# Kernel optimization log

Measured on AMD Instinct MI355X. Metric: run time of the kernel, lower is better.

## Reference

```python
import jax, jax.numpy as jnp
import numpy as np

B, J, HID, INTER, NL = 4096, 16, 128, 64, 4
NEG = -9.0e15
EDGES = [(0,1),(1,2),(2,3),(0,4),(4,5),(5,6),(0,7),(7,8),(8,9),(8,10),(10,11),(11,12),(8,13),(13,14),(14,15)]
GROUPED = [0,7,1,4,2,5,3,6,8,10,9,13,11,14,12,15]  # flattened nodes_group


def _adjacency_nonzeros():
    A = np.zeros((J, J), np.float32)
    for i, j in EDGES:
        A[i, j] = 1.0
        A[j, i] = 1.0
    A += np.eye(J, dtype=np.float32)
    rows, cols = np.nonzero(A)  # row-major, matches torch adj[mask] = e fill order
    return rows.astype(np.int32), cols.astype(np.int32)


def setup_inputs() -> dict:
    key = jax.random.key(0)
    ks = iter(jax.random.split(key, 64))
    rn = lambda shape, s: jax.random.normal(next(ks), shape, jnp.float32) * s
    rows, cols = _adjacency_nonzeros()
    nnz = rows.shape[0]  # 46
    inp = dict(
        x=jax.random.normal(next(ks), (B, J, 2), jnp.float32),
        # input SemGraphConv (2 -> HID) + its BatchNorm
        gc_in_W=rn((2, 2, HID), 0.7), gc_in_e=1.0 + rn((nnz,), 0.3), gc_in_b=rn((HID,), 0.05),
        bn_in_g=1.0 + rn((HID,), 0.05), bn_in_b=rn((HID,), 0.05),
        # 4 residual blocks x 2 graph convs (HID -> HID)
        W_res=rn((2 * NL, 2, HID, HID), 0.08), e_res=1.0 + rn((2 * NL, nnz), 0.3),
        b_res=rn((2 * NL, HID), 0.05),
        bng_res=1.0 + rn((2 * NL, HID), 0.05), bnb_res=rn((2 * NL, HID), 0.05),
        # 5 GraphNonLocal blocks (1 after input + 1 per residual block)
        nl_g_w=rn((NL + 1, INTER, HID), 0.08), nl_g_b=rn((NL + 1, INTER), 0.05),
        nl_t_w=rn((NL + 1, INTER, HID), 0.08), nl_t_b=rn((NL + 1, INTER), 0.05),
        nl_p_w=rn((NL + 1, INTER, HID), 0.08), nl_p_b=rn((NL + 1, INTER), 0.05),
        nl_cp_w=rn((NL + 1, 2 * INTER), 0.08),  # concat_project 1x1 conv, no bias
        nl_W_w=rn((NL + 1, HID, INTER), 0.08), nl_W_b=rn((NL + 1, HID), 0.05),
        nl_bn_g=1.0 + rn((NL + 1, HID), 0.05), nl_bn_b=rn((NL + 1, HID), 0.05),
        # output SemGraphConv (HID -> 3)
        gc_out_W=rn((2, HID, 3), 0.08), gc_out_e=1.0 + rn((nnz,), 0.3), gc_out_b=rn((3,), 0.05),
        # integer constants
        mask_rows=jnp.asarray(rows), mask_cols=jnp.asarray(cols),
        grouped_order=jnp.asarray(GROUPED, jnp.int32),
        restored_order=jnp.asarray(np.argsort(GROUPED), jnp.int32),
    )
    return inp


def reference(x, gc_in_W, gc_in_e, gc_in_b, bn_in_g, bn_in_b,
              W_res, e_res, b_res, bng_res, bnb_res,
              nl_g_w, nl_g_b, nl_t_w, nl_t_b, nl_p_w, nl_p_b,
              nl_cp_w, nl_W_w, nl_W_b, nl_bn_g, nl_bn_b,
              gc_out_W, gc_out_e, gc_out_b,
              mask_rows, mask_cols, grouped_order, restored_order):
    eye = jnp.eye(J, dtype=x.dtype)

    def gconv(h, W, e, b):
        # h: [B, J, F]
        h0 = jnp.einsum('bjf,fo->bjo', h, W[0])
        h1 = jnp.einsum('bjf,fo->bjo', h, W[1])
        logits = jnp.full((J, J), NEG, h.dtype).at[mask_rows, mask_cols].set(e)
        adj = jax.nn.softmax(logits, axis=1)
        diag = jnp.diagonal(adj)                     # adj*I picks diagonal scaling
        off = adj * (1.0 - eye)
        return diag[None, :, None] * h0 + jnp.einsum('ij,bjo->bio', off, h1) + b

    def bn(h, g, bta, axes):
        # training-mode BatchNorm (biased variance), per-channel
        m = h.mean(axes, keepdims=True)
        v = h.var(axes, keepdims=True)
        return (h - m) * jax.lax.rsqrt(v + 1e-5) * g + bta

    def graph_conv(h, W, e, b, gm, gb):
        h = gconv(h, W, e, b)
        h = bn(h, gm[None, None, :], gb[None, None, :], (0, 1))
        return jax.nn.relu(h)

    def nonlocal_block(h, i):
        xo = h[:, grouped_order]          # [B, J, C] regroup joints
        xc = xo.transpose(0, 2, 1)        # [B, C, J]
        conv = lambda w, bb: jnp.einsum('oc,bcj->boj', w, xc) + bb[None, :, None]
        pool = lambda t: t.reshape(B, INTER, J // 2, 2).max(-1)   # MaxPool1d(k=2)
        gx = pool(conv(nl_g_w[i], nl_g_b[i]))                     # [B, I, J/2]
        th = conv(nl_t_w[i], nl_t_b[i])                           # [B, I, J]
        ph = pool(conv(nl_p_w[i], nl_p_b[i]))                     # [B, I, J/2]
        wt, wp = nl_cp_w[i][:INTER], nl_cp_w[i][INTER:]
        # concat_project 1x1 conv over concat(theta,phi) decomposes into a sum
        f = jax.nn.relu(jnp.einsum('bch,c->bh', th, wt)[:, :, None]
                        + jnp.einsum('bcw,c->bw', ph, wp)[:, None, :])  # [B, J, J/2]
        f = f / (J // 2)
        y = jnp.einsum('bhw,bcw->bch', f, gx)                     # [B, I, J]
        Wy = jnp.einsum('oc,bch->boh', nl_W_w[i], y) + nl_W_b[i][None, :, None]
        Wy = bn(Wy, nl_bn_g[i][None, :, None], nl_bn_b[i][None, :, None], (0, 2))
        z = Wy + xc
        return z.transpose(0, 2, 1)[:, restored_order]

    out = graph_conv(x, gc_in_W, gc_in_e, gc_in_b, bn_in_g, bn_in_b)
    out = nonlocal_block(out, 0)
    for i in range(NL):
        res = out
        out = graph_conv(out, W_res[2 * i], e_res[2 * i], b_res[2 * i], bng_res[2 * i], bnb_res[2 * i])
        out = graph_conv(out, W_res[2 * i + 1], e_res[2 * i + 1], b_res[2 * i + 1], bng_res[2 * i + 1], bnb_res[2 * i + 1])
        out = res + out
        out = nonlocal_block(out, i + 1)
    return gconv(out, gc_out_W, gc_out_e, gc_out_b)  # [B, J, 3]
```

## Files before the change

kernel.cpp:

```cpp
#include <hip/hip_runtime.h>

#define B 4096
#define J 16
#define HID 128
#define INTER 64
#define NLAYERS 4
#define NEGV -9000000000000000.0f
#define ELEMS ((size_t)B*16*128)
#define NREP 16
#define SLOT 4096

typedef __attribute__((ext_vector_type(8))) short short8;
typedef __attribute__((ext_vector_type(4))) float f32x4;

static __device__ __forceinline__ unsigned short f2bf(float x) {
    unsigned u = __float_as_uint(x);
    unsigned r = u + 0x7fffu + ((u >> 16) & 1u);
    return (unsigned short)(r >> 16);
}
static __device__ __forceinline__ void splitbf(float x, unsigned short& h, unsigned short& l) {
    h = f2bf(x);
    float hf = __uint_as_float((unsigned)h << 16);
    l = f2bf(x - hf);
}
static __device__ __forceinline__ void splitbf4(float4 v, uint2& hh, uint2& ll) {
    unsigned short h0,l0,h1,l1,h2,l2,h3,l3;
    splitbf(v.x,h0,l0); splitbf(v.y,h1,l1); splitbf(v.z,h2,l2); splitbf(v.w,h3,l3);
    hh = make_uint2((unsigned)h0 | ((unsigned)h1<<16), (unsigned)h2 | ((unsigned)h3<<16));
    ll = make_uint2((unsigned)l0 | ((unsigned)l1<<16), (unsigned)l2 | ((unsigned)l3<<16));
}
static __device__ __forceinline__ f32x4 mfma16(short8 a, short8 b, f32x4 c) {
    return __builtin_amdgcn_mfma_f32_16x16x32_bf16(a, b, c, 0, 0, 0);
}
static __device__ __forceinline__ f32x4 mfma_split(short8 ah, short8 al,
                                                   short8 bh, short8 bl, f32x4 acc) {
    acc = mfma16(ah, bh, acc);
    acc = mfma16(ah, bl, acc);
    acc = mfma16(al, bh, acc);
    return acc;
}
static __device__ __forceinline__ float bfpair(unsigned short h, unsigned short l) {
    return __uint_as_float((unsigned)h << 16) + __uint_as_float((unsigned)l << 16);
}

__global__ void adj_kernel(const float* __restrict__ e_in,
                           const float* __restrict__ e_res,
                           const float* __restrict__ e_out,
                           const int* __restrict__ rows,
                           const int* __restrict__ cols, int nnz,
                           float* __restrict__ off_all,
                           float* __restrict__ diag_all) {
    int m = blockIdx.x;
    int i = threadIdx.x;
    const float* e = (m == 0) ? e_in : (m <= 8) ? e_res + (size_t)(m - 1) * nnz : e_out;
    float l[16];
    for (int j = 0; j < 16; j++) l[j] = NEGV;
    for (int k = 0; k < nnz; k++)
        if (rows[k] == i) l[cols[k]] = e[k];
    float mx = l[0];
    for (int j = 1; j < 16; j++) mx = fmaxf(mx, l[j]);
    float ex[16], s = 0.f;
    for (int j = 0; j < 16; j++) { ex[j] = expf(l[j] - mx); s += ex[j]; }
    float inv = 1.f / s;
    for (int j = 0; j < 16; j++) {
        float a = ex[j] * inv;
        if (j == i) { diag_all[m * 16 + i] = a; a = 0.f; }
        off_all[m * 256 + i * 16 + j] = a;
    }
}

#define WB_N   262144
#define NLW_N  122880
#define NLWW_N 40960
__global__ void prep_w_kernel(const float* __restrict__ W_res,
                              const float* __restrict__ g_w, const float* __restrict__ t_w,
                              const float* __restrict__ p_w, const float* __restrict__ W_w,
                              unsigned short* __restrict__ Wbh, unsigned short* __restrict__ Wbl,
                              unsigned short* __restrict__ nlwh, unsigned short* __restrict__ nlwl,
                              unsigned short* __restrict__ nlWh, unsigned short* __restrict__ nlWl) {
    int i = blockIdx.x * 256 + threadIdx.x;
    unsigned short h, l;
    if (i < WB_N) {
        int lay = i >> 15, rem = i & 32767, n = rem >> 8, k = rem & 255;
        int d = k >> 7, f = k & 127;
        splitbf(W_res[(((lay << 1) | d) * 128 + f) * 128 + n], h, l);
        Wbh[i] = h; Wbl[i] = l;
    } else if (i < WB_N + NLW_N) {
        int j = i - WB_N;
        int lay = j / 24576, r2 = j % 24576;
        int conv = r2 >> 13, oc = r2 & 8191;
        const float* src = conv == 0 ? g_w : conv == 1 ? t_w : p_w;
        splitbf(src[lay * 8192 + oc], h, l);
        nlwh[j] = h; nlwl[j] = l;
    } else if (i < WB_N + NLW_N + NLWW_N) {
        int j = i - WB_N - NLW_N;
        splitbf(W_w[j], h, l);
        nlWh[j] = h; nlWl[j] = l;
    }
}

__global__ void prep_vt_kernel(const float* __restrict__ t_w, const float* __restrict__ t_b,
                               const float* __restrict__ cp_w,
                               float* __restrict__ vt, float* __restrict__ ct) {
    int l = blockIdx.x, c = threadIdx.x;
    float s = 0.f;
    for (int c2 = 0; c2 < 64; c2++)
        s += cp_w[l * 128 + c2] * t_w[(l * 64 + c2) * 128 + c];
    vt[l * 128 + c] = s;
    if (c == 0) {
        float s2 = 0.f;
        for (int c2 = 0; c2 < 64; c2++) s2 += cp_w[l * 128 + c2] * t_b[l * 64 + c2];
        ct[l] = s2;
    }
}

__global__ void finalize_kernel(const float* __restrict__ slot, float* __restrict__ fin) {
    __shared__ float sh[256];
    int t = threadIdx.x;
    float s = 0.f;
    #pragma unroll
    for (int r = 0; r < NREP; r++) s += slot[r * 256 + t];
    sh[t] = s;
    __syncthreads();
    if (t < 128) {
        float m = sh[t] * (1.f / 65536.f);
        float v = sh[128 + t] * (1.f / 65536.f) - m * m;
        fin[t] = m;
        fin[128 + t] = rsqrtf(v + 1e-5f);
    }
}

__global__ __launch_bounds__(256) void gconv_in_kernel(
        const float* __restrict__ x, const float* __restrict__ W,
        const float* __restrict__ bias, const float* __restrict__ off,
        const float* __restrict__ diag, float* __restrict__ out,
        float* __restrict__ stats_out) {
    __shared__ float xs[16][2];
    __shared__ float gs[16][2];
    __shared__ float red[512];
    int b = blockIdx.x, t = threadIdx.x;
    if (t < 32) xs[t >> 1][t & 1] = x[b * 32 + t];
    __syncthreads();
    if (t < 32) {
        int i = t >> 1, f = t & 1;
        float g = 0.f;
        #pragma unroll
        for (int j = 0; j < 16; j++) g += off[i * 16 + j] * xs[j][f];
        gs[i][f] = g;
    }
    __syncthreads();
    int o = t & 127;
    float w00 = W[o], w01 = W[128 + o], w10 = W[256 + o], w11 = W[384 + o], bo = bias[o];
    float s = 0.f, q = 0.f;
    for (int idx = t; idx < 2048; idx += 256) {
        int i = idx >> 7;
        float v = diag[i] * (xs[i][0] * w00 + xs[i][1] * w01)
                + gs[i][0] * w10 + gs[i][1] * w11 + bo;
        out[(size_t)b * 2048 + idx] = v;
        s += v; q += v * v;
    }
    red[t] = s; red[256 + t] = q;
    __syncthreads();
    float* so = stats_out + (b & (NREP - 1)) * 256;
    if (t < 128) {
        atomicAdd(&so[t], red[t] + red[t + 128]);
        atomicAdd(&so[128 + t], red[256 + t] + red[256 + t + 128]);
    }
}

__global__ __launch_bounds__(256) void gconv_mfma_kernel(
        const float* src, const float* wy,
        const float* __restrict__ fin,
        const float* __restrict__ bn_g, const float* __restrict__ bn_b,
        const int* __restrict__ restored, float* zdst,
        const unsigned short* __restrict__ Wbh,
        const unsigned short* __restrict__ Wbl,
        const float* __restrict__ bias,
        const float* __restrict__ off, const float* __restrict__ diag,
        float* dst, float* __restrict__ stats_out) {
    __shared__ float hraw[16][132];
    __shared__ __align__(16) unsigned short ksh[16][264];
    __shared__ __align__(16) unsigned short ksl[16][264];
    __shared__ float offs[256];
    __shared__ float diags[16];
    int t = threadIdx.x;
    offs[t] = off[t];
    if (t < 16) diags[t] = diag[t];
    int c4 = (4 * t) & 127;
    int r0 = t >> 5;
    float4 m4 = make_float4(0,0,0,0), sc4 = make_float4(0,0,0,0), bb4 = make_float4(0,0,0,0);
    if (fin) {
        m4 = *(const float4*)&fin[c4];
        float4 iv = *(const float4*)&fin[128 + c4];
        float4 g4 = *(const float4*)&bn_g[c4];
        bb4 = *(const float4*)&bn_b[c4];
        sc4 = make_float4(iv.x * g4.x, iv.y * g4.y, iv.z * g4.z, iv.w * g4.w);
    }
    int ro0 = 0, ro1 = 0;
    if (wy) { ro0 = restored[r0]; ro1 = restored[r0 + 8]; }
    int b0 = blockIdx.x;
    const float4* src4 = (const float4*)src;
    const float4* wy4  = (const float4*)wy;
    float4 sv0 = src4[(size_t)b0 * 512 + t];
    float4 sv1 = src4[(size_t)b0 * 512 + 256 + t];
    float4 wv0 = make_float4(0,0,0,0), wv1 = make_float4(0,0,0,0);
    if (wy) {
        wv0 = wy4[(size_t)b0 * 512 + ro0 * 32 + (c4 >> 2)];
        wv1 = wy4[(size_t)b0 * 512 + ro1 * 32 + (c4 >> 2)];
    }
    int wv_ = t >> 6, lane = t & 63;
    int mn = lane & 15, kq = (lane >> 4) << 3, qr = (lane >> 4) << 2;

    for (int s = 0; s < 2; s++) {
        int bb_ = blockIdx.x + s * 2048;
        {
            float4 v = sv0;
            if (wy) {
                v.x += (wv0.x - m4.x) * sc4.x + bb4.x;
                v.y += (wv0.y - m4.y) * sc4.y + bb4.y;
                v.z += (wv0.z - m4.z) * sc4.z + bb4.z;
                v.w += (wv0.w - m4.w) * sc4.w + bb4.w;
                ((float4*)zdst)[(size_t)bb_ * 512 + t] = v;
            } else if (fin) {
                v.x = fmaxf((v.x - m4.x) * sc4.x + bb4.x, 0.f);
                v.y = fmaxf((v.y - m4.y) * sc4.y + bb4.y, 0.f);
                v.z = fmaxf((v.z - m4.z) * sc4.z + bb4.z, 0.f);
                v.w = fmaxf((v.w - m4.w) * sc4.w + bb4.w, 0.f);
            }
            *(float4*)&hraw[r0][c4] = v;
            v = sv1;
            if (wy) {
                v.x += (wv1.x - m4.x) * sc4.x + bb4.x;
                v.y += (wv1.y - m4.y) * sc4.y + bb4.y;
                v.z += (wv1.z - m4.z) * sc4.z + bb4.z;
                v.w += (wv1.w - m4.w) * sc4.w + bb4.w;
                ((float4*)zdst)[(size_t)bb_ * 512 + 256 + t] = v;
            } else if (fin) {
                v.x = fmaxf((v.x - m4.x) * sc4.x + bb4.x, 0.f);
                v.y = fmaxf((v.y - m4.y) * sc4.y + bb4.y, 0.f);
                v.z = fmaxf((v.z - m4.z) * sc4.z + bb4.z, 0.f);
                v.w = fmaxf((v.w - m4.w) * sc4.w + bb4.w, 0.f);
            }
            *(float4*)&hraw[r0 + 8][c4] = v;
        }
        if (s == 0) {
            int b1 = blockIdx.x + 2048;
            sv0 = src4[(size_t)b1 * 512 + t];
            sv1 = src4[(size_t)b1 * 512 + 256 + t];
            if (wy) {
                wv0 = wy4[(size_t)b1 * 512 + ro0 * 32 + (c4 >> 2)];
                wv1 = wy4[(size_t)b1 * 512 + ro1 * 32 + (c4 >> 2)];
            }
        }
        __syncthreads();
        for (int u = t; u < 512; u += 256) {
            int i = u >> 5, f4 = (u & 31) << 2;
            float4 hv = *(const float4*)&hraw[i][f4];
            float4 g = make_float4(0.f, 0.f, 0.f, 0.f);
            #pragma unroll
            for (int j = 0; j < 16; j++) {
                float w = offs[i * 16 + j];
                float4 hj = *(const float4*)&hraw[j][f4];
                g.x += w * hj.x; g.y += w * hj.y; g.z += w * hj.z; g.w += w * hj.w;
            }
            float d = diags[i];
            uint2 hh, ll;
            splitbf4(make_float4(d * hv.x, d * hv.y, d * hv.z, d * hv.w), hh, ll);
            *(uint2*)&ksh[i][f4] = hh;
            *(uint2*)&ksl[i][f4] = ll;
            splitbf4(g, hh, ll);
            *(uint2*)&ksh[i][128 + f4] = hh;
            *(uint2*)&ksl[i][128 + f4] = ll;
        }
        __syncthreads();
        int n0 = wv_ << 5;
        f32x4 acc0 = {0.f, 0.f, 0.f, 0.f}, acc1 = {0.f, 0.f, 0.f, 0.f};
        const unsigned short* wh0 = Wbh + (size_t)(n0 + mn) * 256 + kq;
        const unsigned short* wl0 = Wbl + (size_t)(n0 + mn) * 256 + kq;
        #pragma unroll
        for (int k = 0; k < 8; k++) {
            int k0 = k << 5;
            short8 ah = *(const short8*)&ksh[mn][k0 + kq];
            short8 al = *(const short8*)&ksl[mn][k0 + kq];
            acc0 = mfma_split(ah, al, *(const short8*)(wh0 + k0), *(const short8*)(wl0 + k0), acc0);
            acc1 = mfma_split(ah, al, *(const short8*)(wh0 + 4096 + k0), *(const short8*)(wl0 + 4096 + k0), acc1);
        }
        float bias0 = bias[n0 + mn], bias1 = bias[n0 + 16 + mn];
        float s0 = 0.f, q0 = 0.f, s1 = 0.f, q1 = 0.f;
        #pragma unroll
        for (int r = 0; r < 4; r++) {
            int row = qr + r;
            float v0 = acc0[r] + bias0;
            float v1 = acc1[r] + bias1;
            dst[(size_t)bb_ * 2048 + row * 128 + n0 + mn] = v0;
            dst[(size_t)bb_ * 2048 + row * 128 + n0 + 16 + mn] = v1;
            s0 += v0; q0 += v0 * v0; s1 += v1; q1 += v1 * v1;
        }
        s0 += __shfl_xor(s0, 16); s0 += __shfl_xor(s0, 32);
        q0 += __shfl_xor(q0, 16); q0 += __shfl_xor(q0, 32);
        s1 += __shfl_xor(s1, 16); s1 += __shfl_xor(s1, 32);
        q1 += __shfl_xor(q1, 16); q1 += __shfl_xor(q1, 32);
        float* so = stats_out + (bb_ & (NREP - 1)) * 256;
        if (lane < 16) {
            atomicAdd(&so[n0 + mn], s0);
            atomicAdd(&so[128 + n0 + mn], q0);
            atomicAdd(&so[n0 + 16 + mn], s1);
            atomicAdd(&so[128 + n0 + 16 + mn], q1);
        }
        if (s == 0) __syncthreads();
    }
}

#define CG(conv, o, j) cgbuf[((conv) * 64 + (o)) * 17 + (j)]
#define WYL(o, j)      cgbuf[(o) * 17 + (j)]
__global__ __launch_bounds__(512) void nl_a_kernel(
        const float* tsrc, const float* __restrict__ fin,
        const float* __restrict__ bn_g, const float* __restrict__ bn_b,
        const float* res,
        const unsigned short* __restrict__ nlwh,
        const unsigned short* __restrict__ nlwl,
        const float* __restrict__ g_b, const float* __restrict__ p_b,
        const float* __restrict__ cpw,
        const float* __restrict__ vt, const float* __restrict__ ctp,
        const unsigned short* __restrict__ nlWh,
        const unsigned short* __restrict__ nlWl,
        const float* __restrict__ W_b,
        const int* __restrict__ restored,
        float* hdst, float* wydst, float* __restrict__ wst) {
    __shared__ __align__(16) unsigned short xch[16][136];
    __shared__ __align__(16) unsigned short xcl[16][136];
    __shared__ float cgbuf[2176];
    __shared__ float gx[64][9];
    __shared__ float tvp[16][4], pvp[8][8];
    __shared__ float tv[16], pv[8];
    __shared__ float vtl[128];
    __shared__ __align__(16) unsigned short ybh[16][72];
    __shared__ __align__(16) unsigned short ybl[16][72];
    __shared__ float redS[512], redQ[512];
    int b = blockIdx.x, t = threadIdx.x;
    {
        if (t < 128) vtl[t] = vt[t];
        int c4 = (4 * t) & 127;
        int r = t >> 5;
        float4 m4 = *(const float4*)&fin[c4];
        float4 iv = *(const float4*)&fin[128 + c4];
        float4 g4 = *(const float4*)&bn_g[c4];
        float4 bb4 = *(const float4*)&bn_b[c4];
        float4 sc4 = make_float4(iv.x * g4.x, iv.y * g4.y, iv.z * g4.z, iv.w * g4.w);
        float4 v = ((const float4*)tsrc)[(size_t)b * 512 + t];
        v.x = fmaxf((v.x - m4.x) * sc4.x + bb4.x, 0.f);
        v.y = fmaxf((v.y - m4.y) * sc4.y + bb4.y, 0.f);
        v.z = fmaxf((v.z - m4.z) * sc4.z + bb4.z, 0.f);
        v.w = fmaxf((v.w - m4.w) * sc4.w + bb4.w, 0.f);
        if (res) {
            float4 rv = ((const float4*)res)[(size_t)b * 512 + t];
            v.x += rv.x; v.y += rv.y; v.z += rv.z; v.w += rv.w;
        }
        ((float4*)hdst)[(size_t)b * 512 + t] = v;
        int rg = restored[r];
        uint2 hh, ll;
        splitbf4(v, hh, ll);
        *(uint2*)&xch[rg][c4] = hh;
        *(uint2*)&xcl[rg][c4] = ll;
    }
    __syncthreads();
    int w = t >> 6, lane = t & 63;
    int mn = lane & 15, kq = (lane >> 4) << 3, qr = (lane >> 4) << 2;
    {
        int conv = w >> 2;
        int mt = w & 3;
        int wbase = (conv == 0) ? 0 : 128;
        const unsigned short* aph = nlwh + (size_t)(wbase + mt * 16 + mn) * 128 + kq;
        const unsigned short* apl = nlwl + (size_t)(wbase + mt * 16 + mn) * 128 + kq;
        f32x4 acc = {0.f, 0.f, 0.f, 0.f};
        #pragma unroll
        for (int k = 0; k < 4; k++) {
            short8 bh = *(const short8*)&xch[mn][k * 32 + kq];
            short8 bl = *(const short8*)&xcl[mn][k * 32 + kq];
            acc = mfma_split(*(const short8*)(aph + k * 32), *(const short8*)(apl + k * 32),
                             bh, bl, acc);
        }
        const float* bias = (conv == 0) ? g_b : p_b;
        #pragma unroll
        for (int r = 0; r < 4; r++) {
            int o = mt * 16 + qr + r;
            CG(conv, o, mn) = acc[r] + bias[o];
        }
    }
    __syncthreads();
    {
        int c = t >> 3, w2 = t & 7;
        gx[c][w2] = fmaxf(CG(0, c, 2 * w2), CG(0, c, 2 * w2 + 1));
        if (t < 64) {
            int w2b = t & 7, ch = t >> 3;
            float ss = 0.f;
            for (int cc = ch * 8; cc < ch * 8 + 8; cc++)
                ss += fmaxf(CG(1, cc, 2 * w2b), CG(1, cc, 2 * w2b + 1)) * cpw[64 + cc];
            pvp[w2b][ch] = ss;
        } else if (t < 128) {
            int u = t - 64, j = u & 15, ch = u >> 4;
            float ss = 0.f;
            int c0 = ch * 32;
            for (int cc = c0; cc < c0 + 32; cc += 2) {
                unsigned hh = *(const unsigned*)&xch[j][cc];
                unsigned ll = *(const unsigned*)&xcl[j][cc];
                float v0 = bfpair((unsigned short)hh, (unsigned short)ll);
                float v1 = bfpair((unsigned short)(hh >> 16), (unsigned short)(ll >> 16));
                ss += vtl[cc] * v0 + vtl[cc + 1] * v1;
            }
            tvp[j][ch] = ss;
        }
    }
    __syncthreads();
    if (t < 16) {
        tv[t] = tvp[t][0] + tvp[t][1] + tvp[t][2] + tvp[t][3] + ctp[0];
    } else if (t < 24) {
        int w2 = t - 16;
        float ss = 0.f;
        #pragma unroll
        for (int ch = 0; ch < 8; ch++) ss += pvp[w2][ch];
        pv[w2] = ss;
    }
    __syncthreads();
    #pragma unroll
    for (int u2 = 0; u2 < 2; u2++) {
        int u = t + u2 * 512;
        int j = u >> 6, c = u & 63;
        float ss = 0.f;
        #pragma unroll
        for (int w2 = 0; w2 < 8; w2++)
            ss += fmaxf(tv[j] + pv[w2], 0.f) * gx[c][w2];
        unsigned short h, l;
        splitbf(ss * 0.125f, h, l);
        ybh[j][c] = h; ybl[j][c] = l;
    }
    __syncthreads();
    {
        int mt = w;
        short8 byh0 = *(const short8*)&ybh[mn][kq];
        short8 byh1 = *(const short8*)&ybh[mn][32 + kq];
        short8 byl0 = *(const short8*)&ybl[mn][kq];
        short8 byl1 = *(const short8*)&ybl[mn][32 + kq];
        const unsigned short* aph = nlWh + (size_t)(mt * 16 + mn) * 64 + kq;
        const unsigned short* apl = nlWl + (size_t)(mt * 16 + mn) * 64 + kq;
        f32x4 acc = {0.f, 0.f, 0.f, 0.f};
        acc = mfma_split(*(const short8*)aph, *(const short8*)apl, byh0, byl0, acc);
        acc = mfma_split(*(const short8*)(aph + 32), *(const short8*)(apl + 32), byh1, byl1, acc);
        #pragma unroll
        for (int r = 0; r < 4; r++) {
            int o = mt * 16 + qr + r;
            WYL(o, mn) = acc[r] + W_b[o];
        }
    }
    __syncthreads();
    {
        int c = t & 127;
        float ss = 0.f, qq = 0.f;
        #pragma unroll
        for (int u2 = 0; u2 < 4; u2++) {
            int idx = t + u2 * 512;
            int j = idx >> 7;
            float v = WYL(c, j);
            wydst[(size_t)b * 2048 + idx] = v;
            ss += v; qq += v * v;
        }
        redS[t] = ss; redQ[t] = qq;
        __syncthreads();
        float* so = wst + (b & (NREP - 1)) * 256;
        if (t < 128) {
            float s4 = redS[t] + redS[t + 128] + redS[t + 256] + redS[t + 384];
            float q4 = redQ[t] + redQ[t + 128] + redQ[t + 256] + redQ[t + 384];
            atomicAdd(&so[t], s4);
            atomicAdd(&so[128 + t], q4);
        }
    }
}

__global__ __launch_bounds__(256) void gconv_out_kernel(
        const float* __restrict__ h, const float* __restrict__ wy,
        const float* __restrict__ fin,
        const float* __restrict__ nlg, const float* __restrict__ nlb,
        const int* __restrict__ restored,
        const float* __restrict__ W,
        const float* __restrict__ bias, const float* __restrict__ off,
        const float* __restrict__ diag, float* __restrict__ out) {
    __shared__ float hs[16][132];
    __shared__ float gsv[16][132];
    __shared__ float offs[256];
    __shared__ float p0[48][4], p1[48][4];
    int b = blockIdx.x, t = threadIdx.x;
    offs[t] = off[t];
    {
        int c = t & 127;
        float mean = fin[c];
        float inv = fin[128 + c] * nlg[c];
        float bb = nlb[c];
        for (int idx = t; idx < 2048; idx += 256) {
            int r = idx >> 7;
            float wval = wy[(size_t)b * 2048 + restored[r] * 128 + c];
            hs[r][c] = (wval - mean) * inv + bb + h[(size_t)b * 2048 + idx];
        }
    }
    __syncthreads();
    for (int idx = t; idx < 2048; idx += 256) {
        int i = idx >> 7, f = idx & 127;
        float g = 0.f;
        #pragma unroll
        for (int j = 0; j < 16; j++) g += offs[i * 16 + j] * hs[j][f];
        gsv[i][f] = g;
    }
    __syncthreads();
    if (t < 192) {
        int oid = t >> 2, chunk = t & 3;
        int i = oid / 3, o = oid % 3;
        float a0 = 0.f, a1 = 0.f;
        int f0 = chunk * 32;
        for (int f = f0; f < f0 + 32; f++) {
            a0 += hs[i][f] * W[f * 3 + o];
            a1 += gsv[i][f] * W[384 + f * 3 + o];
        }
        p0[oid][chunk] = a0; p1[oid][chunk] = a1;
    }
    __syncthreads();
    if (t < 48) {
        int i = t / 3, o = t % 3;
        float a0 = p0[t][0] + p0[t][1] + p0[t][2] + p0[t][3];
        float a1 = p1[t][0] + p1[t][1] + p1[t][2] + p1[t][3];
        out[(size_t)b * 48 + t] = diag[i] * a0 + a1 + bias[o];
    }
}

extern "C" void kernel_launch(void* const* d_in, const int* in_sizes, int n_in,
                              void* d_out, int out_size, void* d_ws, size_t ws_size,
                              hipStream_t stream) {
    (void)n_in; (void)out_size; (void)ws_size;
    const float* x        = (const float*)d_in[0];
    const float* gc_in_W  = (const float*)d_in[1];
    const float* gc_in_e  = (const float*)d_in[2];
    const float* gc_in_b  = (const float*)d_in[3];
    const float* bn_in_g  = (const float*)d_in[4];
    const float* bn_in_b  = (const float*)d_in[5];
    const float* W_res    = (const float*)d_in[6];
    const float* e_res    = (const float*)d_in[7];
    const float* b_res    = (const float*)d_in[8];
    const float* bng_res  = (const float*)d_in[9];
    const float* bnb_res  = (const float*)d_in[10];
    const float* nl_g_w   = (const float*)d_in[11];
    const float* nl_g_b   = (const float*)d_in[12];
    const float* nl_t_w   = (const float*)d_in[13];
    const float* nl_t_b   = (const float*)d_in[14];
    const float* nl_p_w   = (const float*)d_in[15];
    const float* nl_p_b   = (const float*)d_in[16];
    const float* nl_cp_w  = (const float*)d_in[17];
    const float* nl_W_w   = (const float*)d_in[18];
    const float* nl_W_b   = (const float*)d_in[19];
    const float* nl_bn_g  = (const float*)d_in[20];
    const float* nl_bn_b  = (const float*)d_in[21];
    const float* gc_out_W = (const float*)d_in[22];
    const float* gc_out_e = (const float*)d_in[23];
    const float* gc_out_b = (const float*)d_in[24];
    const int*   mask_rows = (const int*)d_in[25];
    const int*   mask_cols = (const int*)d_in[26];
    const int*   restored  = (const int*)d_in[28];
    int nnz = in_sizes[2];

    float* ws       = (float*)d_ws;
    float* off_all  = ws;
    float* diag_all = ws + 2560;
    float* stats    = ws + 2720;
    float* fin      = ws + 60064;
    float* vt       = ws + 63664;
    float* ct       = ws + 64304;
    unsigned short* Wbh  = (unsigned short*)(ws + 65536);
    unsigned short* Wbl  = Wbh + WB_N;
    unsigned short* nlwh = Wbl + WB_N;
    unsigned short* nlwl = nlwh + NLW_N;
    unsigned short* nlWh = nlwl + NLW_N;
    unsigned short* nlWl = nlWh + NLWW_N;
    float* Z = ws + 491520;
    float* T = Z + ELEMS;

    hipMemsetAsync(stats, 0, 14 * SLOT * sizeof(float), stream);
    adj_kernel<<<10, 16, 0, stream>>>(gc_in_e, e_res, gc_out_e, mask_rows, mask_cols,
                                      nnz, off_all, diag_all);
    prep_w_kernel<<<(WB_N + NLW_N + NLWW_N + 255) / 256, 256, 0, stream>>>(
        W_res, nl_g_w, nl_t_w, nl_p_w, nl_W_w, Wbh, Wbl, nlwh, nlwl, nlWh, nlWl);
    prep_vt_kernel<<<5, 128, 0, stream>>>(nl_t_w, nl_t_b, nl_cp_w, vt, ct);

    gconv_in_kernel<<<B, 256, 0, stream>>>(x, gc_in_W, gc_in_b, off_all, diag_all,
                                           T, stats);
    finalize_kernel<<<1, 256, 0, stream>>>(stats, fin);
    nl_a_kernel<<<B, 512, 0, stream>>>(T, fin, bn_in_g, bn_in_b, nullptr,
                                       nlwh, nlwl, nl_g_b, nl_p_b, nl_cp_w,
                                       vt, ct, nlWh, nlWl, nl_W_b, restored,
                                       Z, T, stats + SLOT);
    finalize_kernel<<<1, 256, 0, stream>>>(stats + SLOT, fin + 256);

    int sl = 1;
    for (int i = 0; i < NLAYERS; i++) {
        int l0 = 2 * i, l1 = 2 * i + 1, li = i + 1;
        gconv_mfma_kernel<<<2048, 256, 0, stream>>>(
            Z, T, fin + (size_t)sl * 256,
            nl_bn_g + i * 128, nl_bn_b + i * 128, restored, Z,
            Wbh + (size_t)l0 * 32768, Wbl + (size_t)l0 * 32768, b_res + l0 * 128,
            off_all + (1 + l0) * 256, diag_all + (1 + l0) * 16, T,
            stats + (size_t)(sl + 1) * SLOT);
        finalize_kernel<<<1, 256, 0, stream>>>(stats + (size_t)(sl + 1) * SLOT,
                                               fin + (size_t)(sl + 1) * 256);
        gconv_mfma_kernel<<<2048, 256, 0, stream>>>(
            T, nullptr, fin + (size_t)(sl + 1) * 256,
            bng_res + l0 * 128, bnb_res + l0 * 128, nullptr, nullptr,
            Wbh + (size_t)l1 * 32768, Wbl + (size_t)l1 * 32768, b_res + l1 * 128,
            off_all + (1 + l1) * 256, diag_all + (1 + l1) * 16, T,
            stats + (size_t)(sl + 2) * SLOT);
        finalize_kernel<<<1, 256, 0, stream>>>(stats + (size_t)(sl + 2) * SLOT,
                                               fin + (size_t)(sl + 2) * 256);
        nl_a_kernel<<<B, 512, 0, stream>>>(
            T, fin + (size_t)(sl + 2) * 256,
            bng_res + l1 * 128, bnb_res + l1 * 128, Z,
            nlwh + li * 24576, nlwl + li * 24576,
            nl_g_b + li * 64, nl_p_b + li * 64, nl_cp_w + li * 128,
            vt + li * 128, ct + li, nlWh + li * 8192, nlWl + li * 8192,
            nl_W_b + li * 128, restored, Z, T,
            stats + (size_t)(sl + 3) * SLOT);
        finalize_kernel<<<1, 256, 0, stream>>>(stats + (size_t)(sl + 3) * SLOT,
                                               fin + (size_t)(sl + 3) * 256);
        sl += 3;
    }
    gconv_out_kernel<<<B, 256, 0, stream>>>(Z, T, fin + (size_t)sl * 256,
                                            nl_bn_g + NLAYERS * 128, nl_bn_b + NLAYERS * 128,
                                            restored, gc_out_W, gc_out_b,
                                            off_all + 9 * 256, diag_all + 9 * 16,
                                            (float*)d_out);
}
```

Before: 901.7 us.

## Process one batch sample per 512-thread block in graph conv kernel

```diff
diff --git a/kernel.cpp b/kernel.cpp
--- a/kernel.cpp
+++ b/kernel.cpp
@@ -168,7 +168,7 @@
     }
 }
 
-__global__ __launch_bounds__(256) void gconv_mfma_kernel(
+__global__ __launch_bounds__(512) void gconv_mfma_kernel(
         const float* src, const float* wy,
         const float* __restrict__ fin,
         const float* __restrict__ bn_g, const float* __restrict__ bn_b,
@@ -183,131 +183,86 @@
     __shared__ __align__(16) unsigned short ksl[16][264];
     __shared__ float offs[256];
     __shared__ float diags[16];
-    int t = threadIdx.x;
-    offs[t] = off[t];
-    if (t < 16) diags[t] = diag[t];
+    int b = blockIdx.x, t = threadIdx.x;
+    if (t < 256) offs[t] = off[t];
+    if (t >= 256 && t < 272) diags[t - 256] = diag[t - 256];
     int c4 = (4 * t) & 127;
     int r0 = t >> 5;
-    float4 m4 = make_float4(0,0,0,0), sc4 = make_float4(0,0,0,0), bb4 = make_float4(0,0,0,0);
-    if (fin) {
-        m4 = *(const float4*)&fin[c4];
-        float4 iv = *(const float4*)&fin[128 + c4];
-        float4 g4 = *(const float4*)&bn_g[c4];
-        bb4 = *(const float4*)&bn_b[c4];
-        sc4 = make_float4(iv.x * g4.x, iv.y * g4.y, iv.z * g4.z, iv.w * g4.w);
-    }
-    int ro0 = 0, ro1 = 0;
-    if (wy) { ro0 = restored[r0]; ro1 = restored[r0 + 8]; }
-    int b0 = blockIdx.x;
-    const float4* src4 = (const float4*)src;
-    const float4* wy4  = (const float4*)wy;
-    float4 sv0 = src4[(size_t)b0 * 512 + t];
-    float4 sv1 = src4[(size_t)b0 * 512 + 256 + t];
-    float4 wv0 = make_float4(0,0,0,0), wv1 = make_float4(0,0,0,0);
-    if (wy) {
-        wv0 = wy4[(size_t)b0 * 512 + ro0 * 32 + (c4 >> 2)];
-        wv1 = wy4[(size_t)b0 * 512 + ro1 * 32 + (c4 >> 2)];
-    }
-    int wv_ = t >> 6, lane = t & 63;
+    {
+        float4 m4 = make_float4(0,0,0,0), sc4 = make_float4(0,0,0,0), bb4 = make_float4(0,0,0,0);
+        if (fin) {
+            m4 = *(const float4*)&fin[c4];
+            float4 iv = *(const float4*)&fin[128 + c4];
+            float4 g4 = *(const float4*)&bn_g[c4];
+            bb4 = *(const float4*)&bn_b[c4];
+            sc4 = make_float4(iv.x * g4.x, iv.y * g4.y, iv.z * g4.z, iv.w * g4.w);
+        }
+        float4 v = ((const float4*)src)[(size_t)b * 512 + t];
+        if (wy) {
+            int ro = restored[r0];
+            float4 wv = ((const float4*)wy)[(size_t)b * 512 + ro * 32 + (c4 >> 2)];
+            v.x += (wv.x - m4.x) * sc4.x + bb4.x;
+            v.y += (wv.y - m4.y) * sc4.y + bb4.y;
+            v.z += (wv.z - m4.z) * sc4.z + bb4.z;
+            v.w += (wv.w - m4.w) * sc4.w + bb4.w;
+            ((float4*)zdst)[(size_t)b * 512 + t] = v;
+        } else if (fin) {
+            v.x = fmaxf((v.x - m4.x) * sc4.x + bb4.x, 0.f);
+            v.y = fmaxf((v.y - m4.y) * sc4.y + bb4.y, 0.f);
+            v.z = fmaxf((v.z - m4.z) * sc4.z + bb4.z, 0.f);
+            v.w = fmaxf((v.w - m4.w) * sc4.w + bb4.w, 0.f);
+        }
+        *(float4*)&hraw[r0][c4] = v;
+    }
+    __syncthreads();
+    {
+        int i = t >> 5, f4 = (t & 31) << 2;
+        float4 hv = *(const float4*)&hraw[i][f4];
+        float4 g = make_float4(0.f, 0.f, 0.f, 0.f);
+        #pragma unroll
+        for (int j = 0; j < 16; j++) {
+            float w = offs[i * 16 + j];
+            float4 hj = *(const float4*)&hraw[j][f4];
+            g.x += w * hj.x; g.y += w * hj.y; g.z += w * hj.z; g.w += w * hj.w;
+        }
+        float d = diags[i];
+        uint2 hh, ll;
+        splitbf4(make_float4(d * hv.x, d * hv.y, d * hv.z, d * hv.w), hh, ll);
+        *(uint2*)&ksh[i][f4] = hh;
+        *(uint2*)&ksl[i][f4] = ll;
+        splitbf4(g, hh, ll);
+        *(uint2*)&ksh[i][128 + f4] = hh;
+        *(uint2*)&ksl[i][128 + f4] = ll;
+    }
+    __syncthreads();
+    int w = t >> 6, lane = t & 63;
     int mn = lane & 15, kq = (lane >> 4) << 3, qr = (lane >> 4) << 2;
-
-    for (int s = 0; s < 2; s++) {
-        int bb_ = blockIdx.x + s * 2048;
-        {
-            float4 v = sv0;
-            if (wy) {
-                v.x += (wv0.x - m4.x) * sc4.x + bb4.x;
-                v.y += (wv0.y - m4.y) * sc4.y + bb4.y;
-                v.z += (wv0.z - m4.z) * sc4.z + bb4.z;
-                v.w += (wv0.w - m4.w) * sc4.w + bb4.w;
-                ((float4*)zdst)[(size_t)bb_ * 512 + t] = v;
-            } else if (fin) {
-                v.x = fmaxf((v.x - m4.x) * sc4.x + bb4.x, 0.f);
-                v.y = fmaxf((v.y - m4.y) * sc4.y + bb4.y, 0.f);
-                v.z = fmaxf((v.z - m4.z) * sc4.z + bb4.z, 0.f);
-                v.w = fmaxf((v.w - m4.w) * sc4.w + bb4.w, 0.f);
-            }
-            *(float4*)&hraw[r0][c4] = v;
-            v = sv1;
-            if (wy) {
-                v.x += (wv1.x - m4.x) * sc4.x + bb4.x;
-                v.y += (wv1.y - m4.y) * sc4.y + bb4.y;
-                v.z += (wv1.z - m4.z) * sc4.z + bb4.z;
-                v.w += (wv1.w - m4.w) * sc4.w + bb4.w;
-                ((float4*)zdst)[(size_t)bb_ * 512 + 256 + t] = v;
-            } else if (fin) {
-                v.x = fmaxf((v.x - m4.x) * sc4.x + bb4.x, 0.f);
-                v.y = fmaxf((v.y - m4.y) * sc4.y + bb4.y, 0.f);
-                v.z = fmaxf((v.z - m4.z) * sc4.z + bb4.z, 0.f);
-                v.w = fmaxf((v.w - m4.w) * sc4.w + bb4.w, 0.f);
-            }
-            *(float4*)&hraw[r0 + 8][c4] = v;
-        }
-        if (s == 0) {
-            int b1 = blockIdx.x + 2048;
-            sv0 = src4[(size_t)b1 * 512 + t];
-            sv1 = src4[(size_t)b1 * 512 + 256 + t];
-            if (wy) {
-                wv0 = wy4[(size_t)b1 * 512 + ro0 * 32 + (c4 >> 2)];
-                wv1 = wy4[(size_t)b1 * 512 + ro1 * 32 + (c4 >> 2)];
-            }
-        }
-        __syncthreads();
-        for (int u = t; u < 512; u += 256) {
-            int i = u >> 5, f4 = (u & 31) << 2;
-            float4 hv = *(const float4*)&hraw[i][f4];
-            float4 g = make_float4(0.f, 0.f, 0.f, 0.f);
-            #pragma unroll
-            for (int j = 0; j < 16; j++) {
-                float w = offs[i * 16 + j];
-                float4 hj = *(const float4*)&hraw[j][f4];
-                g.x += w * hj.x; g.y += w * hj.y; g.z += w * hj.z; g.w += w * hj.w;
-            }
-            float d = diags[i];
-            uint2 hh, ll;
-            splitbf4(make_float4(d * hv.x, d * hv.y, d * hv.z, d * hv.w), hh, ll);
-            *(uint2*)&ksh[i][f4] = hh;
-            *(uint2*)&ksl[i][f4] = ll;
-            splitbf4(g, hh, ll);
-            *(uint2*)&ksh[i][128 + f4] = hh;
-            *(uint2*)&ksl[i][128 + f4] = ll;
-        }
-        __syncthreads();
-        int n0 = wv_ << 5;
-        f32x4 acc0 = {0.f, 0.f, 0.f, 0.f}, acc1 = {0.f, 0.f, 0.f, 0.f};
-        const unsigned short* wh0 = Wbh + (size_t)(n0 + mn) * 256 + kq;
-        const unsigned short* wl0 = Wbl + (size_t)(n0 + mn) * 256 + kq;
-        #pragma unroll
-        for (int k = 0; k < 8; k++) {
-            int k0 = k << 5;
-            short8 ah = *(const short8*)&ksh[mn][k0 + kq];
-            short8 al = *(const short8*)&ksl[mn][k0 + kq];
-            acc0 = mfma_split(ah, al, *(const short8*)(wh0 + k0), *(const short8*)(wl0 + k0), acc0);
-            acc1 = mfma_split(ah, al, *(const short8*)(wh0 + 4096 + k0), *(const short8*)(wl0 + 4096 + k0), acc1);
-        }
-        float bias0 = bias[n0 + mn], bias1 = bias[n0 + 16 + mn];
-        float s0 = 0.f, q0 = 0.f, s1 = 0.f, q1 = 0.f;
-        #pragma unroll
-        for (int r = 0; r < 4; r++) {
-            int row = qr + r;
-            float v0 = acc0[r] + bias0;
-            float v1 = acc1[r] + bias1;
-            dst[(size_t)bb_ * 2048 + row * 128 + n0 + mn] = v0;
-            dst[(size_t)bb_ * 2048 + row * 128 + n0 + 16 + mn] = v1;
-            s0 += v0; q0 += v0 * v0; s1 += v1; q1 += v1 * v1;
-        }
-        s0 += __shfl_xor(s0, 16); s0 += __shfl_xor(s0, 32);
-        q0 += __shfl_xor(q0, 16); q0 += __shfl_xor(q0, 32);
-        s1 += __shfl_xor(s1, 16); s1 += __shfl_xor(s1, 32);
-        q1 += __shfl_xor(q1, 16); q1 += __shfl_xor(q1, 32);
-        float* so = stats_out + (bb_ & (NREP - 1)) * 256;
-        if (lane < 16) {
-            atomicAdd(&so[n0 + mn], s0);
-            atomicAdd(&so[128 + n0 + mn], q0);
-            atomicAdd(&so[n0 + 16 + mn], s1);
-            atomicAdd(&so[128 + n0 + 16 + mn], q1);
-        }
-        if (s == 0) __syncthreads();
+    int n0 = w << 4;
+    f32x4 acc = {0.f, 0.f, 0.f, 0.f};
+    const unsigned short* wh0 = Wbh + (size_t)(n0 + mn) * 256 + kq;
+    const unsigned short* wl0 = Wbl + (size_t)(n0 + mn) * 256 + kq;
+    #pragma unroll
+    for (int k = 0; k < 8; k++) {
+        int k0 = k << 5;
+        short8 ah = *(const short8*)&ksh[mn][k0 + kq];
+        short8 al = *(const short8*)&ksl[mn][k0 + kq];
+        acc = mfma_split(ah, al, *(const short8*)(wh0 + k0), *(const short8*)(wl0 + k0), acc);
+    }
+    float bo = bias[n0 + mn];
+    float s0 = 0.f, q0 = 0.f;
+    #pragma unroll
+    for (int r = 0; r < 4; r++) {
+        int row = qr + r;
+        float v0 = acc[r] + bo;
+        dst[(size_t)b * 2048 + row * 128 + n0 + mn] = v0;
+        s0 += v0; q0 += v0 * v0;
+    }
+    s0 += __shfl_xor(s0, 16); s0 += __shfl_xor(s0, 32);
+    q0 += __shfl_xor(q0, 16); q0 += __shfl_xor(q0, 32);
+    float* so = stats_out + (b & (NREP - 1)) * 256;
+    if (lane < 16) {
+        atomicAdd(&so[n0 + mn], s0);
+        atomicAdd(&so[128 + n0 + mn], q0);
     }
 }
 
@@ -599,7 +554,7 @@
     int sl = 1;
     for (int i = 0; i < NLAYERS; i++) {
         int l0 = 2 * i, l1 = 2 * i + 1, li = i + 1;
-        gconv_mfma_kernel<<<2048, 256, 0, stream>>>(
+        gconv_mfma_kernel<<<B, 512, 0, stream>>>(
             Z, T, fin + (size_t)sl * 256,
             nl_bn_g + i * 128, nl_bn_b + i * 128, restored, Z,
             Wbh + (size_t)l0 * 32768, Wbl + (size_t)l0 * 32768, b_res + l0 * 128,
@@ -607,7 +562,7 @@
             stats + (size_t)(sl + 1) * SLOT);
         finalize_kernel<<<1, 256, 0, stream>>>(stats + (size_t)(sl + 1) * SLOT,
                                                fin + (size_t)(sl + 1) * 256);
-        gconv_mfma_kernel<<<2048, 256, 0, stream>>>(
+        gconv_mfma_kernel<<<B, 512, 0, stream>>>(
             T, nullptr, fin + (size_t)(sl + 1) * 256,
             bng_res + l0 * 128, bnb_res + l0 * 128, nullptr, nullptr,
             Wbh + (size_t)l1 * 32768, Wbl + (size_t)l1 * 32768, b_res + l1 * 128,
```

New measurement: 1.093 ms. +21.3%, slower.

## Process two batch samples per nl_a block with prefetch of the next input

Applied to the files above, without the earlier changes.

```diff
diff --git a/kernel.cpp b/kernel.cpp
--- a/kernel.cpp
+++ b/kernel.cpp
@@ -337,141 +337,152 @@
     __shared__ __align__(16) unsigned short ybh[16][72];
     __shared__ __align__(16) unsigned short ybl[16][72];
     __shared__ float redS[512], redQ[512];
-    int b = blockIdx.x, t = threadIdx.x;
-    {
-        if (t < 128) vtl[t] = vt[t];
-        int c4 = (4 * t) & 127;
-        int r = t >> 5;
-        float4 m4 = *(const float4*)&fin[c4];
-        float4 iv = *(const float4*)&fin[128 + c4];
-        float4 g4 = *(const float4*)&bn_g[c4];
-        float4 bb4 = *(const float4*)&bn_b[c4];
-        float4 sc4 = make_float4(iv.x * g4.x, iv.y * g4.y, iv.z * g4.z, iv.w * g4.w);
-        float4 v = ((const float4*)tsrc)[(size_t)b * 512 + t];
-        v.x = fmaxf((v.x - m4.x) * sc4.x + bb4.x, 0.f);
-        v.y = fmaxf((v.y - m4.y) * sc4.y + bb4.y, 0.f);
-        v.z = fmaxf((v.z - m4.z) * sc4.z + bb4.z, 0.f);
-        v.w = fmaxf((v.w - m4.w) * sc4.w + bb4.w, 0.f);
-        if (res) {
-            float4 rv = ((const float4*)res)[(size_t)b * 512 + t];
-            v.x += rv.x; v.y += rv.y; v.z += rv.z; v.w += rv.w;
-        }
-        ((float4*)hdst)[(size_t)b * 512 + t] = v;
-        int rg = restored[r];
-        uint2 hh, ll;
-        splitbf4(v, hh, ll);
-        *(uint2*)&xch[rg][c4] = hh;
-        *(uint2*)&xcl[rg][c4] = ll;
-    }
-    __syncthreads();
+    int t = threadIdx.x;
+    if (t < 128) vtl[t] = vt[t];
+    int c4 = (4 * t) & 127;
+    int r = t >> 5;
+    int rg = restored[r];
+    float ctv = ctp[0];
+    float4 m4 = *(const float4*)&fin[c4];
+    float4 iv = *(const float4*)&fin[128 + c4];
+    float4 g4 = *(const float4*)&bn_g[c4];
+    float4 bb4 = *(const float4*)&bn_b[c4];
+    float4 sc4 = make_float4(iv.x * g4.x, iv.y * g4.y, iv.z * g4.z, iv.w * g4.w);
     int w = t >> 6, lane = t & 63;
     int mn = lane & 15, kq = (lane >> 4) << 3, qr = (lane >> 4) << 2;
-    {
-        int conv = w >> 2;
-        int mt = w & 3;
-        int wbase = (conv == 0) ? 0 : 128;
-        const unsigned short* aph = nlwh + (size_t)(wbase + mt * 16 + mn) * 128 + kq;
-        const unsigned short* apl = nlwl + (size_t)(wbase + mt * 16 + mn) * 128 + kq;
-        f32x4 acc = {0.f, 0.f, 0.f, 0.f};
+    int b0 = blockIdx.x;
+    float4 sv = ((const float4*)tsrc)[(size_t)b0 * 512 + t];
+    float4 rv = make_float4(0,0,0,0);
+    if (res) rv = ((const float4*)res)[(size_t)b0 * 512 + t];
+
+    for (int s = 0; s < 2; s++) {
+        int b = blockIdx.x + s * 2048;
+        {
+            float4 v = sv;
+            v.x = fmaxf((v.x - m4.x) * sc4.x + bb4.x, 0.f);
+            v.y = fmaxf((v.y - m4.y) * sc4.y + bb4.y, 0.f);
+            v.z = fmaxf((v.z - m4.z) * sc4.z + bb4.z, 0.f);
+            v.w = fmaxf((v.w - m4.w) * sc4.w + bb4.w, 0.f);
+            if (res) { v.x += rv.x; v.y += rv.y; v.z += rv.z; v.w += rv.w; }
+            ((float4*)hdst)[(size_t)b * 512 + t] = v;
+            uint2 hh, ll;
+            splitbf4(v, hh, ll);
+            *(uint2*)&xch[rg][c4] = hh;
+            *(uint2*)&xcl[rg][c4] = ll;
+        }
+        if (s == 0) {
+            int b1 = blockIdx.x + 2048;
+            sv = ((const float4*)tsrc)[(size_t)b1 * 512 + t];
+            if (res) rv = ((const float4*)res)[(size_t)b1 * 512 + t];
+        }
+        __syncthreads();
+        {
+            int conv = w >> 2;
+            int mt = w & 3;
+            int wbase = (conv == 0) ? 0 : 128;
+            const unsigned short* aph = nlwh + (size_t)(wbase + mt * 16 + mn) * 128 + kq;
+            const unsigned short* apl = nlwl + (size_t)(wbase + mt * 16 + mn) * 128 + kq;
+            f32x4 acc = {0.f, 0.f, 0.f, 0.f};
+            #pragma unroll
+            for (int k = 0; k < 4; k++) {
+                short8 bh = *(const short8*)&xch[mn][k * 32 + kq];
+                short8 bl = *(const short8*)&xcl[mn][k * 32 + kq];
+                acc = mfma_split(*(const short8*)(aph + k * 32), *(const short8*)(apl + k * 32),
+                                 bh, bl, acc);
+            }
+            const float* bias = (conv == 0) ? g_b : p_b;
+            #pragma unroll
+            for (int rr = 0; rr < 4; rr++) {
+                int o = mt * 16 + qr + rr;
+                CG(conv, o, mn) = acc[rr] + bias[o];
+            }
+        }
+        __syncthreads();
+        {
+            int c = t >> 3, w2 = t & 7;
+            gx[c][w2] = fmaxf(CG(0, c, 2 * w2), CG(0, c, 2 * w2 + 1));
+            if (t < 64) {
+                int w2b = t & 7, ch = t >> 3;
+                float ss = 0.f;
+                for (int cc = ch * 8; cc < ch * 8 + 8; cc++)
+                    ss += fmaxf(CG(1, cc, 2 * w2b), CG(1, cc, 2 * w2b + 1)) * cpw[64 + cc];
+                pvp[w2b][ch] = ss;
+            } else if (t < 128) {
+                int u = t - 64, j = u & 15, ch = u >> 4;
+                float ss = 0.f;
+                int c0 = ch * 32;
+                for (int cc = c0; cc < c0 + 32; cc += 2) {
+                    unsigned hh = *(const unsigned*)&xch[j][cc];
+                    unsigned ll = *(const unsigned*)&xcl[j][cc];
+                    float v0 = bfpair((unsigned short)hh, (unsigned short)ll);
+                    float v1 = bfpair((unsigned short)(hh >> 16), (unsigned short)(ll >> 16));
+                    ss += vtl[cc] * v0 + vtl[cc + 1] * v1;
+                }
+                tvp[j][ch] = ss;
+            }
+        }
+        __syncthreads();
+        if (t < 16) {
+            tv[t] = tvp[t][0] + tvp[t][1] + tvp[t][2] + tvp[t][3] + ctv;
+        } else if (t < 24) {
+            int w2 = t - 16;
+            float ss = 0.f;
+            #pragma unroll
+            for (int ch = 0; ch < 8; ch++) ss += pvp[w2][ch];
+            pv[w2] = ss;
+        }
+        __syncthreads();
         #pragma unroll
-        for (int k = 0; k < 4; k++) {
-            short8 bh = *(const short8*)&xch[mn][k * 32 + kq];
-            short8 bl = *(const short8*)&xcl[mn][k * 32 + kq];
-            acc = mfma_split(*(const short8*)(aph + k * 32), *(const short8*)(apl + k * 32),
-                             bh, bl, acc);
-        }
-        const float* bias = (conv == 0) ? g_b : p_b;
-        #pragma unroll
-        for (int r = 0; r < 4; r++) {
-            int o = mt * 16 + qr + r;
-            CG(conv, o, mn) = acc[r] + bias[o];
-        }
-    }
-    __syncthreads();
-    {
-        int c = t >> 3, w2 = t & 7;
-        gx[c][w2] = fmaxf(CG(0, c, 2 * w2), CG(0, c, 2 * w2 + 1));
-        if (t < 64) {
-            int w2b = t & 7, ch = t >> 3;
+        for (int u2 = 0; u2 < 2; u2++) {
+            int u = t + u2 * 512;
+            int j = u >> 6, c = u & 63;
             float ss = 0.f;
-            for (int cc = ch * 8; cc < ch * 8 + 8; cc++)
-                ss += fmaxf(CG(1, cc, 2 * w2b), CG(1, cc, 2 * w2b + 1)) * cpw[64 + cc];
-            pvp[w2b][ch] = ss;
-        } else if (t < 128) {
-            int u = t - 64, j = u & 15, ch = u >> 4;
-            float ss = 0.f;
-            int c0 = ch * 32;
-            for (int cc = c0; cc < c0 + 32; cc += 2) {
-                unsigned hh = *(const unsigned*)&xch[j][cc];
-                unsigned ll = *(const unsigned*)&xcl[j][cc];
-                float v0 = bfpair((unsigned short)hh, (unsigned short)ll);
-                float v1 = bfpair((unsigned short)(hh >> 16), (unsigned short)(ll >> 16));
-                ss += vtl[cc] * v0 + vtl[cc + 1] * v1;
-            }
-            tvp[j][ch] = ss;
-        }
-    }
-    __syncthreads();
-    if (t < 16) {
-        tv[t] = tvp[t][0] + tvp[t][1] + tvp[t][2] + tvp[t][3] + ctp[0];
-    } else if (t < 24) {
-        int w2 = t - 16;
-        float ss = 0.f;
-        #pragma unroll
-        for (int ch = 0; ch < 8; ch++) ss += pvp[w2][ch];
-        pv[w2] = ss;
-    }
-    __syncthreads();
-    #pragma unroll
-    for (int u2 = 0; u2 < 2; u2++) {
-        int u = t + u2 * 512;
-        int j = u >> 6, c = u & 63;
-        float ss = 0.f;
-        #pragma unroll
-        for (int w2 = 0; w2 < 8; w2++)
-            ss += fmaxf(tv[j] + pv[w2], 0.f) * gx[c][w2];
-        unsigned short h, l;
-        splitbf(ss * 0.125f, h, l);
-        ybh[j][c] = h; ybl[j][c] = l;
-    }
-    __syncthreads();
-    {
-        int mt = w;
-        short8 byh0 = *(const short8*)&ybh[mn][kq];
-        short8 byh1 = *(const short8*)&ybh[mn][32 + kq];
-        short8 byl0 = *(const short8*)&ybl[mn][kq];
-        short8 byl1 = *(const short8*)&ybl[mn][32 + kq];
-        const unsigned short* aph = nlWh + (size_t)(mt * 16 + mn) * 64 + kq;
-        const unsigned short* apl = nlWl + (size_t)(mt * 16 + mn) * 64 + kq;
-        f32x4 acc = {0.f, 0.f, 0.f, 0.f};
-        acc = mfma_split(*(const short8*)aph, *(const short8*)apl, byh0, byl0, acc);
-        acc = mfma_split(*(const short8*)(aph + 32), *(const short8*)(apl + 32), byh1, byl1, acc);
-        #pragma unroll
-        for (int r = 0; r < 4; r++) {
-            int o = mt * 16 + qr + r;
-            WYL(o, mn) = acc[r] + W_b[o];
-        }
-    }
-    __syncthreads();
-    {
-        int c = t & 127;
-        float ss = 0.f, qq = 0.f;
-        #pragma unroll
-        for (int u2 = 0; u2 < 4; u2++) {
-            int idx = t + u2 * 512;
-            int j = idx >> 7;
-            float v = WYL(c, j);
-            wydst[(size_t)b * 2048 + idx] = v;
-            ss += v; qq += v * v;
-        }
-        redS[t] = ss; redQ[t] = qq;
-        __syncthreads();
-        float* so = wst + (b & (NREP - 1)) * 256;
-        if (t < 128) {
-            float s4 = redS[t] + redS[t + 128] + redS[t + 256] + redS[t + 384];
-            float q4 = redQ[t] + redQ[t + 128] + redQ[t + 256] + redQ[t + 384];
-            atomicAdd(&so[t], s4);
-            atomicAdd(&so[128 + t], q4);
+            #pragma unroll
+            for (int w2 = 0; w2 < 8; w2++)
+                ss += fmaxf(tv[j] + pv[w2], 0.f) * gx[c][w2];
+            unsigned short h, l;
+            splitbf(ss * 0.125f, h, l);
+            ybh[j][c] = h; ybl[j][c] = l;
+        }
+        __syncthreads();
+        {
+            int mt = w;
+            short8 byh0 = *(const short8*)&ybh[mn][kq];
+            short8 byh1 = *(const short8*)&ybh[mn][32 + kq];
+            short8 byl0 = *(const short8*)&ybl[mn][kq];
+            short8 byl1 = *(const short8*)&ybl[mn][32 + kq];
+            const unsigned short* aph = nlWh + (size_t)(mt * 16 + mn) * 64 + kq;
+            const unsigned short* apl = nlWl + (size_t)(mt * 16 + mn) * 64 + kq;
+            f32x4 acc = {0.f, 0.f, 0.f, 0.f};
+            acc = mfma_split(*(const short8*)aph, *(const short8*)apl, byh0, byl0, acc);
+            acc = mfma_split(*(const short8*)(aph + 32), *(const short8*)(apl + 32), byh1, byl1, acc);
+            #pragma unroll
+            for (int rr = 0; rr < 4; rr++) {
+                int o = mt * 16 + qr + rr;
+                WYL(o, mn) = acc[rr] + W_b[o];
+            }
+        }
+        __syncthreads();
+        {
+            int c = t & 127;
+            float ss = 0.f, qq = 0.f;
+            #pragma unroll
+            for (int u2 = 0; u2 < 4; u2++) {
+                int idx = t + u2 * 512;
+                int j = idx >> 7;
+                float v = WYL(c, j);
+                wydst[(size_t)b * 2048 + idx] = v;
+                ss += v; qq += v * v;
+            }
+            redS[t] = ss; redQ[t] = qq;
+            __syncthreads();
+            float* so = wst + (b & (NREP - 1)) * 256;
+            if (t < 128) {
+                float s4 = redS[t] + redS[t + 128] + redS[t + 256] + redS[t + 384];
+                float q4 = redQ[t] + redQ[t + 128] + redQ[t + 256] + redQ[t + 384];
+                atomicAdd(&so[t], s4);
+                atomicAdd(&so[128 + t], q4);
+            }
         }
     }
 }
@@ -590,10 +601,10 @@
     gconv_in_kernel<<<B, 256, 0, stream>>>(x, gc_in_W, gc_in_b, off_all, diag_all,
                                            T, stats);
     finalize_kernel<<<1, 256, 0, stream>>>(stats, fin);
-    nl_a_kernel<<<B, 512, 0, stream>>>(T, fin, bn_in_g, bn_in_b, nullptr,
-                                       nlwh, nlwl, nl_g_b, nl_p_b, nl_cp_w,
-                                       vt, ct, nlWh, nlWl, nl_W_b, restored,
-                                       Z, T, stats + SLOT);
+    nl_a_kernel<<<2048, 512, 0, stream>>>(T, fin, bn_in_g, bn_in_b, nullptr,
+                                          nlwh, nlwl, nl_g_b, nl_p_b, nl_cp_w,
+                                          vt, ct, nlWh, nlWl, nl_W_b, restored,
+                                          Z, T, stats + SLOT);
     finalize_kernel<<<1, 256, 0, stream>>>(stats + SLOT, fin + 256);
 
     int sl = 1;
@@ -615,7 +626,7 @@
             stats + (size_t)(sl + 2) * SLOT);
         finalize_kernel<<<1, 256, 0, stream>>>(stats + (size_t)(sl + 2) * SLOT,
                                                fin + (size_t)(sl + 2) * 256);
-        nl_a_kernel<<<B, 512, 0, stream>>>(
+        nl_a_kernel<<<2048, 512, 0, stream>>>(
             T, fin + (size_t)(sl + 2) * 256,
             bng_res + l1 * 128, bnb_res + l1 * 128, Z,
             nlwh + li * 24576, nlwl + li * 24576,
```

Result: no change. 919.0 us (+1.9%).
